# Kernel tuning notes

Hardware: AMD Instinct MI355X
Metric: run time of the kernel (lower is better)

## Reference

```python
import jax, jax.numpy as jnp
import numpy as np

B, S, D, H, H2 = 2048, 96, 7, 64, 16  # batch, seq, input/output feat, bilstm hidden, lstm2 hidden


def setup_inputs() -> dict:
    key = jax.random.key(0)
    ks = jax.random.split(key, 32)
    p = lambda i, shape: jax.random.normal(ks[i], shape, jnp.float32) * 0.1
    inp = {
        'x': jax.random.normal(ks[0], (B, S, D), jnp.float32),
        # feature attention linears (D -> D)
        'fv_w': p(1, (D, D)), 'fv_b': p(2, (D,)),
        'fk_w': p(3, (D, D)), 'fk_b': p(4, (D,)),
        'fq_w': p(5, (D, D)), 'fq_b': p(6, (D,)),
        # bidirectional LSTM, forward dir (torch layout: W_ih [4H,D], W_hh [4H,H])
        'l1f_wih': p(7, (4 * H, D)), 'l1f_whh': p(8, (4 * H, H)),
        'l1f_bih': p(9, (4 * H,)), 'l1f_bhh': p(10, (4 * H,)),
        # backward dir
        'l1b_wih': p(11, (4 * H, D)), 'l1b_whh': p(12, (4 * H, H)),
        'l1b_bih': p(13, (4 * H,)), 'l1b_bhh': p(14, (4 * H,)),
        # temporal attention linears (H -> H)
        'tv_w': p(15, (H, H)), 'tv_b': p(16, (H,)),
        'tk_w': p(17, (H, H)), 'tk_b': p(18, (H,)),
        'tq_w': p(19, (H, H)), 'tq_b': p(20, (H,)),
        # lstm2: input H=64 -> hidden H2=16
        'l2_wih': p(21, (4 * H2, H)), 'l2_whh': p(22, (4 * H2, H2)),
        'l2_bih': p(23, (4 * H2,)), 'l2_bhh': p(24, (4 * H2,)),
        # fc: 16 -> 7
        'fc_w': p(25, (D, H2)), 'fc_b': p(26, (D,)),
    }
    return inp


def _run_lstm(x, wih, whh, bih, bhh, reverse=False):
    # x: [B, S, Din]; torch gate order i, f, g, o
    Hh = whh.shape[1]
    xg = jnp.einsum('bsd,gd->sbg', x, wih) + bih + bhh  # [S, B, 4H]
    h0 = jnp.zeros((x.shape[0], Hh), x.dtype)

    def step(carry, gx):
        h, c = carry
        g = gx + h @ whh.T
        i, f, gg, o = jnp.split(g, 4, axis=-1)
        c = jax.nn.sigmoid(f) * c + jax.nn.sigmoid(i) * jnp.tanh(gg)
        h = jax.nn.sigmoid(o) * jnp.tanh(c)
        return (h, c), h

    _, hs = jax.lax.scan(step, (h0, h0), xg, reverse=reverse)
    return jnp.swapaxes(hs, 0, 1)  # [B, S, H]


def _fwd(x, fv_w, fv_b, fk_w, fk_b, fq_w, fq_b,
         l1f_wih, l1f_whh, l1f_bih, l1f_bhh,
         l1b_wih, l1b_whh, l1b_bih, l1b_bhh,
         tv_w, tv_b, tk_w, tk_b, tq_w, tq_b,
         l2_wih, l2_whh, l2_bih, l2_bhh, fc_w, fc_b):
    lin = lambda y, w, b: y @ w.T + b
    # feature attention (over the D=7 feature axis)
    v = lin(x, fv_w, fv_b)
    k = lin(x + v, fk_w, fk_b)
    q = lin(x + k, fq_w, fq_b)
    fatt = jax.nn.softmax(jnp.einsum('bsi,bsj->bij', q, k), axis=-1)  # [B, D, D]
    fa = jnp.tanh(jnp.einsum('bsi,bij->bsj', v, fatt) + x)
    # bidirectional LSTM; concat-view-mean over directions == (hf + hb) / 2
    hf = _run_lstm(fa, l1f_wih, l1f_whh, l1f_bih, l1f_bhh, reverse=False)
    hb = _run_lstm(fa, l1b_wih, l1b_whh, l1b_bih, l1b_bhh, reverse=True)
    lo = 0.5 * (hf + hb)  # [B, S, H]
    # temporal attention (over the S axis)
    tv = lin(lo, tv_w, tv_b)
    tk = lin(lo, tk_w, tk_b)
    tq = lin(lo, tq_w, tq_b)
    tatt = jax.nn.softmax(jnp.einsum('bid,bjd->bij', tq, tk), axis=-1)  # [B, S, S]
    to = jnp.tanh(jnp.einsum('bij,bjd->bid', tatt, tv))
    # second LSTM + fc
    o2 = _run_lstm(to, l2_wih, l2_whh, l2_bih, l2_bhh, reverse=False)  # [B, S, 16]
    return o2 @ fc_w.T + fc_b  # [B, S, D]


def reference(x, fv_w, fv_b, fk_w, fk_b, fq_w, fq_b,
              l1f_wih, l1f_whh, l1f_bih, l1f_bhh,
              l1b_wih, l1b_whh, l1b_bih, l1b_bhh,
              tv_w, tv_b, tk_w, tk_b, tq_w, tq_b,
              l2_wih, l2_whh, l2_bih, l2_bhh, fc_w, fc_b):
    return _fwd(x, fv_w, fv_b, fk_w, fk_b, fq_w, fq_b,
                l1f_wih, l1f_whh, l1f_bih, l1f_bhh,
                l1b_wih, l1b_whh, l1b_bih, l1b_bhh,
                tv_w, tv_b, tk_w, tk_b, tq_w, tq_b,
                l2_wih, l2_whh, l2_bih, l2_bhh, fc_w, fc_b)
```

## Files before the change

### kernel.cpp

```cpp
#include <hip/hip_runtime.h>
#include <math.h>

#define BB 2048
#define SS 96
#define DD 7
#define HH 64
#define H2 16
#define FASTR 776
#define HST2 72
#define LOST2 88
#define KST 120
#define HSB 20

typedef _Float16 f16x8 __attribute__((ext_vector_type(8)));
typedef _Float16 f16x4 __attribute__((ext_vector_type(4)));
typedef float f32x4 __attribute__((ext_vector_type(4)));

__device__ __forceinline__ float frcp(float x) { return __builtin_amdgcn_rcpf(x); }
__device__ __forceinline__ float sigm(float x) { return frcp(1.0f + __expf(-x)); }
__device__ __forceinline__ float tanh_f(float x) { return 1.0f - 2.0f * frcp(__expf(2.0f * x) + 1.0f); }
__device__ __forceinline__ float rl(float v, int l) {
    return __int_as_float(__builtin_amdgcn_readlane(__float_as_int(v), l));
}
__device__ __forceinline__ f16x8 frag_from_f32(const float* base) {
    const float4* p = (const float4*)base;
    float4 a = p[0], b = p[1];
    f16x8 r;
    r[0] = (_Float16)a.x; r[1] = (_Float16)a.y; r[2] = (_Float16)a.z; r[3] = (_Float16)a.w;
    r[4] = (_Float16)b.x; r[5] = (_Float16)b.y; r[6] = (_Float16)b.z; r[7] = (_Float16)b.w;
    return r;
}

__global__ __launch_bounds__(256) void k_feat(
    const float* __restrict__ x,
    const float* __restrict__ fv_w, const float* __restrict__ fv_b,
    const float* __restrict__ fk_w, const float* __restrict__ fk_b,
    const float* __restrict__ fq_w, const float* __restrict__ fq_b,
    float* __restrict__ fa_out)
{
    __shared__ float xs[SS * DD], vs[SS * DD], ks[SS * DD], qs[SS * DD];
    __shared__ float att[DD * DD];
    __shared__ float wv[DD * DD], wk[DD * DD], wq[DD * DD];
    __shared__ float bv[DD], bk[DD], bq[DD];
    const int b = blockIdx.x, t = threadIdx.x;
    const float* xb = x + (size_t)b * SS * DD;

    for (int idx = t; idx < SS * DD; idx += 256) xs[idx] = xb[idx];
    if (t < DD * DD) { wv[t] = fv_w[t]; wk[t] = fk_w[t]; wq[t] = fq_w[t]; }
    if (t < DD)      { bv[t] = fv_b[t]; bk[t] = fk_b[t]; bq[t] = fq_b[t]; }
    __syncthreads();

    for (int idx = t; idx < SS * DD; idx += 256) {
        int s = idx / DD, j = idx % DD;
        float a = bv[j];
        #pragma unroll
        for (int i = 0; i < DD; i++) a += xs[s * DD + i] * wv[j * DD + i];
        vs[idx] = a;
    }
    __syncthreads();
    for (int idx = t; idx < SS * DD; idx += 256) {
        int s = idx / DD, j = idx % DD;
        float a = bk[j];
        #pragma unroll
        for (int i = 0; i < DD; i++) a += (xs[s * DD + i] + vs[s * DD + i]) * wk[j * DD + i];
        ks[idx] = a;
    }
    __syncthreads();
    for (int idx = t; idx < SS * DD; idx += 256) {
        int s = idx / DD, j = idx % DD;
        float a = bq[j];
        #pragma unroll
        for (int i = 0; i < DD; i++) a += (xs[s * DD + i] + ks[s * DD + i]) * wq[j * DD + i];
        qs[idx] = a;
    }
    __syncthreads();
    if (t < DD * DD) {
        int i = t / DD, j = t % DD;
        float a = 0.0f;
        for (int s = 0; s < SS; s++) a += qs[s * DD + i] * ks[s * DD + j];
        att[t] = a;
    }
    __syncthreads();
    if (t < DD) {
        float m = -1e30f;
        #pragma unroll
        for (int j = 0; j < DD; j++) m = fmaxf(m, att[t * DD + j]);
        float e[DD]; float sum = 0.0f;
        #pragma unroll
        for (int j = 0; j < DD; j++) { e[j] = __expf(att[t * DD + j] - m); sum += e[j]; }
        float inv = frcp(sum);
        #pragma unroll
        for (int j = 0; j < DD; j++) att[t * DD + j] = e[j] * inv;
    }
    __syncthreads();
    for (int idx = t; idx < SS * DD; idx += 256) {
        int s = idx / DD, j = idx % DD;
        float a = xs[idx];
        #pragma unroll
        for (int i = 0; i < DD; i++) a += vs[s * DD + i] * att[i * DD + j];
        fa_out[(size_t)b * SS * DD + idx] = tanh_f(a);
    }
}

__global__ __launch_bounds__(256, 2) void k_bilstm(
    const float* __restrict__ fa,
    const float* __restrict__ wih_f, const float* __restrict__ whh_f,
    const float* __restrict__ bih_f, const float* __restrict__ bhh_f,
    const float* __restrict__ wih_b, const float* __restrict__ whh_b,
    const float* __restrict__ bih_b, const float* __restrict__ bhh_b,
    _Float16* __restrict__ hf, _Float16* __restrict__ hb)
{
    __shared__ _Float16 faS[16 * FASTR];
    __shared__ _Float16 hS[2][16 * HST2];

    const int bx = blockIdx.x;
    const int bg = bx >> 1, dir = bx & 1;
    const int t = threadIdx.x, lane = t & 63, w = t >> 6;
    const int col = lane & 15, quad = lane >> 4;

    const float* wih = dir ? wih_b : wih_f;
    const float* whh = dir ? whh_b : whh_f;
    const float* bih = dir ? bih_b : bih_f;
    const float* bhh = dir ? bhh_b : bhh_f;
    _Float16* hout = dir ? hb : hf;

    for (int i = t; i < 2 * 16 * HST2 / 2; i += 256) ((unsigned int*)hS)[i] = 0u;

    f16x8 wh[4][2];
    f16x8 wi[4];
    #pragma unroll
    for (int gt = 0; gt < 4; gt++) {
        const int row = 16 * (w + 4 * gt) + col;
        wh[gt][0] = frag_from_f32(whh + row * HH + quad * 8);
        wh[gt][1] = frag_from_f32(whh + row * HH + 32 + quad * 8);
        f16x8 v;
        #pragma unroll
        for (int j = 0; j < 8; j++) v[j] = (_Float16)0.0f;
        if (quad == 0) {
            #pragma unroll
            for (int j = 0; j < DD; j++) v[j] = (_Float16)wih[row * DD + j];
            v[7] = (_Float16)(bih[row] + bhh[row]);
        }
        wi[gt] = v;
    }

    const float* fab = fa + (size_t)(bg * 16) * SS * DD;
    for (int idx = t; idx < 16 * SS * DD; idx += 256) {
        int n = idx / (SS * DD), r = idx % (SS * DD);
        int s = r / DD, i = r % DD;
        faS[n * FASTR + s * 8 + i] = (_Float16)fab[idx];
    }
    for (int idx = t; idx < 16 * SS; idx += 256) {
        int n = idx / SS, s = idx % SS;
        faS[n * FASTR + s * 8 + 7] = (_Float16)1.0f;
    }
    __syncthreads();

    const int sstep = dir ? -HH : HH;
    _Float16* hp = hout + ((size_t)(bg * 16 + col)) * SS * HH
                 + (dir ? (SS - 1) : 0) * HH + 16 * w + quad * 4;

    const f32x4 ZC = {0.f, 0.f, 0.f, 0.f};
    float c0 = 0.f, c1 = 0.f, c2 = 0.f, c3 = 0.f;
    f16x4 hq;
    f32x4 gin[4];

    {
        const int s0 = dir ? (SS - 1) : 0;
        f16x8 faf;
        #pragma unroll
        for (int j = 0; j < 8; j++) faf[j] = (_Float16)0.0f;
        if (quad == 0) faf = *(const f16x8*)(&faS[col * FASTR + s0 * 8]);
        #pragma unroll
        for (int gt = 0; gt < 4; gt++)
            gin[gt] = __builtin_amdgcn_mfma_f32_16x16x32_f16(wi[gt], faf, ZC, 0, 0, 0);
    }

    for (int step = 0; step < SS; step++) {
        const int p = step & 1;

        if (step) {
            *(f16x4*)hp = hq;
            hp += sstep;
        }

        f16x8 h0 = *(const f16x8*)(&hS[p][col * HST2 + quad * 8]);
        f16x8 h1 = *(const f16x8*)(&hS[p][col * HST2 + 32 + quad * 8]);

        f32x4 g[4];
        #pragma unroll
        for (int gt = 0; gt < 4; gt++) {
            f32x4 acc = __builtin_amdgcn_mfma_f32_16x16x32_f16(wh[gt][0], h0, gin[gt], 0, 0, 0);
            acc = __builtin_amdgcn_mfma_f32_16x16x32_f16(wh[gt][1], h1, acc, 0, 0, 0);
            g[gt] = acc;
        }
        {
            float iv, fv, gv, ov, hv;
            iv = sigm(g[0][0]); fv = sigm(g[1][0]); gv = tanh_f(g[2][0]); ov = sigm(g[3][0]);
            c0 = fv * c0 + iv * gv; hv = ov * tanh_f(c0); hq[0] = (_Float16)hv;
            iv = sigm(g[0][1]); fv = sigm(g[1][1]); gv = tanh_f(g[2][1]); ov = sigm(g[3][1]);
            c1 = fv * c1 + iv * gv; hv = ov * tanh_f(c1); hq[1] = (_Float16)hv;
            iv = sigm(g[0][2]); fv = sigm(g[1][2]); gv = tanh_f(g[2][2]); ov = sigm(g[3][2]);
            c2 = fv * c2 + iv * gv; hv = ov * tanh_f(c2); hq[2] = (_Float16)hv;
            iv = sigm(g[0][3]); fv = sigm(g[1][3]); gv = tanh_f(g[2][3]); ov = sigm(g[3][3]);
            c3 = fv * c3 + iv * gv; hv = ov * tanh_f(c3); hq[3] = (_Float16)hv;
        }
        *(f16x4*)(&hS[1 - p][col * HST2 + 16 * w + quad * 4]) = hq;

        if (step + 1 < SS) {
            const int sn = dir ? (SS - 2 - step) : (step + 1);
            f16x8 faf;
            #pragma unroll
            for (int j = 0; j < 8; j++) faf[j] = (_Float16)0.0f;
            if (quad == 0) faf = *(const f16x8*)(&faS[col * FASTR + sn * 8]);
            #pragma unroll
            for (int gt = 0; gt < 4; gt++)
                gin[gt] = __builtin_amdgcn_mfma_f32_16x16x32_f16(wi[gt], faf, ZC, 0, 0, 0);
        }
        __syncthreads();
    }
    *(f16x4*)hp = hq;
}

__global__ __launch_bounds__(512, 2) void k_attn(
    const _Float16* __restrict__ hf, const _Float16* __restrict__ hb,
    const float* __restrict__ tv_w, const float* __restrict__ tv_b,
    const float* __restrict__ tk_w, const float* __restrict__ tk_b,
    const float* __restrict__ tq_w, const float* __restrict__ tq_b,
    const float* __restrict__ l2_wih,
    const float* __restrict__ l2_bih, const float* __restrict__ l2_bhh,
    _Float16* __restrict__ xg2)
{
    __shared__ _Float16 loB[SS * LOST2];
    __shared__ _Float16 qB[SS * KST];
    __shared__ _Float16 tkS[SS * KST];
    __shared__ _Float16 tvT[HH * KST];

    const int b = blockIdx.x, t = threadIdx.x;
    const int lane = t & 63, w = t >> 6;
    const int col = lane & 15, quad = lane >> 4;

    const _Float16* hfp = hf + (size_t)b * SS * HH;
    const _Float16* hbp = hb + (size_t)b * SS * HH;
    for (int g8 = t; g8 < 768; g8 += 512) {
        f16x8 va = *(const f16x8*)(hfp + g8 * 8);
        f16x8 vb = *(const f16x8*)(hbp + g8 * 8);
        int s = g8 >> 3, d = (g8 & 7) * 8;
        f16x8 r;
        #pragma unroll
        for (int j = 0; j < 8; j++) r[j] = (_Float16)(0.5f * ((float)va[j] + (float)vb[j]));
        *(f16x8*)(&loB[s * LOST2 + d]) = r;
    }
    __syncthreads();

    for (int i = 0; i < 9; i++) {
        const int flat = w + 8 * i;
        const int proj = flat / 24, rem = flat % 24;
        const int mt = rem >> 2, nt = rem & 3;
        const float* wmat = (proj == 0) ? tv_w : (proj == 1) ? tk_w : tq_w;
        const float* bvec = (proj == 0) ? tv_b : (proj == 1) ? tk_b : tq_b;
        const int j = 16 * nt + col;
        f32x4 acc = {0.f, 0.f, 0.f, 0.f};
        #pragma unroll
        for (int kc = 0; kc < 2; kc++) {
            f16x8 a  = *(const f16x8*)(&loB[(16 * mt + col) * LOST2 + kc * 32 + quad * 8]);
            f16x8 bb = frag_from_f32(wmat + j * HH + kc * 32 + quad * 8);
            acc = __builtin_amdgcn_mfma_f32_16x16x32_f16(a, bb, acc, 0, 0, 0);
        }
        const float bj = bvec[j];
        #pragma unroll
        for (int r = 0; r < 4; r++) {
            const float v = acc[r] + bj;
            const int row = 16 * mt + quad * 4 + r;
            if (proj == 0)      tvT[j * KST + row] = (_Float16)v;
            else if (proj == 1) tkS[row * KST + j] = (_Float16)v;
            else                qB[row * KST + j]  = (_Float16)v;
        }
    }
    __syncthreads();

    if (w < 6) {
        const int mt = w;
        f16x8 aq0 = *(const f16x8*)(qB + (16 * mt + col) * KST + quad * 8);
        f16x8 aq1 = *(const f16x8*)(qB + (16 * mt + col) * KST + 32 + quad * 8);
        f32x4 sc[6];
        #pragma unroll
        for (int nt = 0; nt < 6; nt++) {
            f32x4 acc = {0.f, 0.f, 0.f, 0.f};
            f16x8 b0 = *(const f16x8*)(tkS + (16 * nt + col) * KST + quad * 8);
            f16x8 b1 = *(const f16x8*)(tkS + (16 * nt + col) * KST + 32 + quad * 8);
            acc = __builtin_amdgcn_mfma_f32_16x16x32_f16(aq0, b0, acc, 0, 0, 0);
            acc = __builtin_amdgcn_mfma_f32_16x16x32_f16(aq1, b1, acc, 0, 0, 0);
            sc[nt] = acc;
        }
        #pragma unroll
        for (int r = 0; r < 4; r++) {
            float m = sc[0][r];
            #pragma unroll
            for (int nt = 1; nt < 6; nt++) m = fmaxf(m, sc[nt][r]);
            #pragma unroll
            for (int o = 1; o < 16; o <<= 1) m = fmaxf(m, __shfl_xor(m, o));
            float e[6]; float sum = 0.0f;
            #pragma unroll
            for (int nt = 0; nt < 6; nt++) { e[nt] = __expf(sc[nt][r] - m); sum += e[nt]; }
            #pragma unroll
            for (int o = 1; o < 16; o <<= 1) sum += __shfl_xor(sum, o);
            const float inv = frcp(sum);
            const int row = 16 * mt + quad * 4 + r;
            #pragma unroll
            for (int nt = 0; nt < 6; nt++)
                qB[row * KST + 16 * nt + col] = (_Float16)(e[nt] * inv);
        }
        f16x8 pa0 = *(const f16x8*)(qB + (16 * mt + col) * KST + quad * 8);
        f16x8 pa1 = *(const f16x8*)(qB + (16 * mt + col) * KST + 32 + quad * 8);
        f16x8 pa2 = *(const f16x8*)(qB + (16 * mt + col) * KST + 64 + quad * 8);
        #pragma unroll
        for (int nt = 0; nt < 4; nt++) {
            f32x4 acc = {0.f, 0.f, 0.f, 0.f};
            const _Float16* tvrow = tvT + (16 * nt + col) * KST;
            acc = __builtin_amdgcn_mfma_f32_16x16x32_f16(pa0, *(const f16x8*)(tvrow + quad * 8), acc, 0, 0, 0);
            acc = __builtin_amdgcn_mfma_f32_16x16x32_f16(pa1, *(const f16x8*)(tvrow + 32 + quad * 8), acc, 0, 0, 0);
            acc = __builtin_amdgcn_mfma_f32_16x16x32_f16(pa2, *(const f16x8*)(tvrow + 64 + quad * 8), acc, 0, 0, 0);
            #pragma unroll
            for (int r = 0; r < 4; r++)
                loB[(16 * mt + quad * 4 + r) * LOST2 + 16 * nt + col] = (_Float16)tanh_f(acc[r]);
        }
    }
    __syncthreads();

    for (int i = 0; i < 3; i++) {
        const int flat = w + 8 * i;
        const int mt = flat >> 2, nt = flat & 3;
        const int g = 16 * nt + col;
        f32x4 acc = {0.f, 0.f, 0.f, 0.f};
        #pragma unroll
        for (int kc = 0; kc < 2; kc++) {
            f16x8 a  = *(const f16x8*)(&loB[(16 * mt + col) * LOST2 + kc * 32 + quad * 8]);
            f16x8 bb = frag_from_f32(l2_wih + g * HH + kc * 32 + quad * 8);
            acc = __builtin_amdgcn_mfma_f32_16x16x32_f16(a, bb, acc, 0, 0, 0);
        }
        const float bg2 = l2_bih[g] + l2_bhh[g];
        #pragma unroll
        for (int r = 0; r < 4; r++) {
            const int row = 16 * mt + quad * 4 + r;
            xg2[(size_t)b * SS * HH + row * HH + g] = (_Float16)(acc[r] + bg2);
        }
    }
}

__global__ __launch_bounds__(256) void k_lstm2(
    const _Float16* __restrict__ xg2,
    const float* __restrict__ l2_whh,
    const float* __restrict__ fc_w, const float* __restrict__ fc_b,
    float* __restrict__ out)
{
    __shared__ _Float16 hsb[4][SS * HSB];

    const int t = threadIdx.x, lane = t & 63, w = t >> 6;
    const int n = blockIdx.x * 4 + w;
    const int u16 = lane & 15;

    float whr[H2];
    #pragma unroll
    for (int j = 0; j < H2; j++) whr[j] = l2_whh[lane * H2 + j];

    const _Float16* xgp = xg2 + (size_t)n * SS * HH + lane;
    float h = 0.0f, c = 0.0f;
    _Float16 xv = xgp[0];

    for (int s = 0; s < SS; s++) {
        _Float16 xnext = (_Float16)0.0f;
        if (s + 1 < SS) xnext = xgp[(s + 1) * HH];

        float a = (float)xv;
        #pragma unroll
        for (int j = 0; j < H2; j++) a += rl(h, j) * whr[j];
        float iv = __shfl(a, u16);
        float fv = __shfl(a, H2 + u16);
        float gv = __shfl(a, 2 * H2 + u16);
        float ov = __shfl(a, 3 * H2 + u16);
        c = sigm(fv) * c + sigm(iv) * tanh_f(gv);
        h = sigm(ov) * tanh_f(c);
        if (lane < H2) hsb[w][s * HSB + lane] = (_Float16)h;
        xv = xnext;
    }
    __syncthreads();

    for (int s = lane; s < SS; s += 64) {
        float hr[H2];
        #pragma unroll
        for (int j = 0; j < H2; j++) hr[j] = (float)hsb[w][s * HSB + j];
        float* op = out + ((size_t)n * SS + s) * DD;
        #pragma unroll
        for (int d = 0; d < DD; d++) {
            float a = fc_b[d];
            #pragma unroll
            for (int j = 0; j < H2; j++) a += hr[j] * fc_w[d * H2 + j];
            op[d] = a;
        }
    }
}

extern "C" void kernel_launch(void* const* d_in, const int* in_sizes, int n_in,
                              void* d_out, int out_size, void* d_ws, size_t ws_size,
                              hipStream_t stream) {
    const float* x     = (const float*)d_in[0];
    const float* fv_w  = (const float*)d_in[1];
    const float* fv_b  = (const float*)d_in[2];
    const float* fk_w  = (const float*)d_in[3];
    const float* fk_b  = (const float*)d_in[4];
    const float* fq_w  = (const float*)d_in[5];
    const float* fq_b  = (const float*)d_in[6];
    const float* l1f_wih = (const float*)d_in[7];
    const float* l1f_whh = (const float*)d_in[8];
    const float* l1f_bih = (const float*)d_in[9];
    const float* l1f_bhh = (const float*)d_in[10];
    const float* l1b_wih = (const float*)d_in[11];
    const float* l1b_whh = (const float*)d_in[12];
    const float* l1b_bih = (const float*)d_in[13];
    const float* l1b_bhh = (const float*)d_in[14];
    const float* tv_w  = (const float*)d_in[15];
    const float* tv_b  = (const float*)d_in[16];
    const float* tk_w  = (const float*)d_in[17];
    const float* tk_b  = (const float*)d_in[18];
    const float* tq_w  = (const float*)d_in[19];
    const float* tq_b  = (const float*)d_in[20];
    const float* l2_wih = (const float*)d_in[21];
    const float* l2_whh = (const float*)d_in[22];
    const float* l2_bih = (const float*)d_in[23];
    const float* l2_bhh = (const float*)d_in[24];
    const float* fc_w  = (const float*)d_in[25];
    const float* fc_b  = (const float*)d_in[26];

    float* fa = (float*)d_ws;
    _Float16* hf = (_Float16*)(fa + (size_t)BB * SS * DD);
    _Float16* hb = hf + (size_t)BB * SS * HH;
    _Float16* xg2 = hf;

    k_feat<<<BB, 256, 0, stream>>>(x, fv_w, fv_b, fk_w, fk_b, fq_w, fq_b, fa);
    k_bilstm<<<256, 256, 0, stream>>>(fa,
        l1f_wih, l1f_whh, l1f_bih, l1f_bhh,
        l1b_wih, l1b_whh, l1b_bih, l1b_bhh, hf, hb);
    k_attn<<<BB, 512, 0, stream>>>(hf, hb,
        tv_w, tv_b, tk_w, tk_b, tq_w, tq_b,
        l2_wih, l2_bih, l2_bhh, xg2);
    k_lstm2<<<512, 256, 0, stream>>>(xg2, l2_whh, fc_w, fc_b, (float*)d_out);
}
```

Before: 297.1 us.

## Use MFMA for LSTM2 recurrence and shrink attention LDS for occupancy

The second LSTM is rewritten so each 64-thread block handles 16 sequences and computes the recurrent gate matmul with 16x16x16 MFMA. Gate inputs are double-buffered in registers, which replaces the per-lane readlane dot products and shuffles of the old one-sequence-per-wave design. In the attention kernel, the Q/K and probability buffers share one LDS region with tighter strides, and an extra barrier makes that aliasing safe; launch bounds are raised to allow more resident blocks per CU. The risks are the extra barrier, possible LDS bank conflicts from the new strides, and much lower parallelism in lstm2, which now launches only 128 single-wave blocks.

```diff
diff --git a/kernel.cpp b/kernel.cpp
--- a/kernel.cpp
+++ b/kernel.cpp
@@ -8,9 +8,11 @@
 #define H2 16
 #define FASTR 776
 #define HST2 72
-#define LOST2 88
-#define KST 120
-#define HSB 20
+#define LO_ST 72
+#define QK_ST 68
+#define TV_ST 104
+#define P_ST 104
+#define HP 20
 
 typedef _Float16 f16x8 __attribute__((ext_vector_type(8)));
 typedef _Float16 f16x4 __attribute__((ext_vector_type(4)));
@@ -28,6 +30,14 @@
     f16x8 r;
     r[0] = (_Float16)a.x; r[1] = (_Float16)a.y; r[2] = (_Float16)a.z; r[3] = (_Float16)a.w;
     r[4] = (_Float16)b.x; r[5] = (_Float16)b.y; r[6] = (_Float16)b.z; r[7] = (_Float16)b.w;
+    return r;
+}
+__device__ __forceinline__ f16x8 ld2x4(const _Float16* p) {
+    f16x4 a = *(const f16x4*)p;
+    f16x4 b = *(const f16x4*)(p + 4);
+    f16x8 r;
+    r[0]=a[0]; r[1]=a[1]; r[2]=a[2]; r[3]=a[3];
+    r[4]=b[0]; r[5]=b[1]; r[6]=b[2]; r[7]=b[3];
     return r;
 }
 
@@ -222,7 +232,7 @@
     *(f16x4*)hp = hq;
 }
 
-__global__ __launch_bounds__(512, 2) void k_attn(
+__global__ __launch_bounds__(512, 6) void k_attn(
     const _Float16* __restrict__ hf, const _Float16* __restrict__ hb,
     const float* __restrict__ tv_w, const float* __restrict__ tv_b,
     const float* __restrict__ tk_w, const float* __restrict__ tk_b,
@@ -231,10 +241,12 @@
     const float* __restrict__ l2_bih, const float* __restrict__ l2_bhh,
     _Float16* __restrict__ xg2)
 {
-    __shared__ _Float16 loB[SS * LOST2];
-    __shared__ _Float16 qB[SS * KST];
-    __shared__ _Float16 tkS[SS * KST];
-    __shared__ _Float16 tvT[HH * KST];
+    __shared__ __align__(16) _Float16 loB[SS * LO_ST];
+    __shared__ __align__(16) _Float16 tvT[HH * TV_ST];
+    __shared__ __align__(16) _Float16 uQK[2 * SS * QK_ST];
+    _Float16* qS  = uQK;
+    _Float16* tkS = uQK + SS * QK_ST;
+    _Float16* pS  = uQK;
 
     const int b = blockIdx.x, t = threadIdx.x;
     const int lane = t & 63, w = t >> 6;
@@ -249,7 +261,7 @@
         f16x8 r;
         #pragma unroll
         for (int j = 0; j < 8; j++) r[j] = (_Float16)(0.5f * ((float)va[j] + (float)vb[j]));
-        *(f16x8*)(&loB[s * LOST2 + d]) = r;
+        *(f16x8*)(&loB[s * LO_ST + d]) = r;
     }
     __syncthreads();
 
@@ -263,7 +275,7 @@
         f32x4 acc = {0.f, 0.f, 0.f, 0.f};
         #pragma unroll
         for (int kc = 0; kc < 2; kc++) {
-            f16x8 a  = *(const f16x8*)(&loB[(16 * mt + col) * LOST2 + kc * 32 + quad * 8]);
+            f16x8 a  = *(const f16x8*)(&loB[(16 * mt + col) * LO_ST + kc * 32 + quad * 8]);
             f16x8 bb = frag_from_f32(wmat + j * HH + kc * 32 + quad * 8);
             acc = __builtin_amdgcn_mfma_f32_16x16x32_f16(a, bb, acc, 0, 0, 0);
         }
@@ -272,27 +284,31 @@
         for (int r = 0; r < 4; r++) {
             const float v = acc[r] + bj;
             const int row = 16 * mt + quad * 4 + r;
-            if (proj == 0)      tvT[j * KST + row] = (_Float16)v;
-            else if (proj == 1) tkS[row * KST + j] = (_Float16)v;
-            else                qB[row * KST + j]  = (_Float16)v;
-        }
-    }
-    __syncthreads();
-
+            if (proj == 0)      tvT[j * TV_ST + row] = (_Float16)v;
+            else if (proj == 1) tkS[row * QK_ST + j] = (_Float16)v;
+            else                qS[row * QK_ST + j]  = (_Float16)v;
+        }
+    }
+    __syncthreads();
+
+    f32x4 sc[6];
+    const int mt = w;
     if (w < 6) {
-        const int mt = w;
-        f16x8 aq0 = *(const f16x8*)(qB + (16 * mt + col) * KST + quad * 8);
-        f16x8 aq1 = *(const f16x8*)(qB + (16 * mt + col) * KST + 32 + quad * 8);
-        f32x4 sc[6];
+        f16x8 aq0 = ld2x4(qS + (16 * mt + col) * QK_ST + quad * 8);
+        f16x8 aq1 = ld2x4(qS + (16 * mt + col) * QK_ST + 32 + quad * 8);
         #pragma unroll
         for (int nt = 0; nt < 6; nt++) {
             f32x4 acc = {0.f, 0.f, 0.f, 0.f};
-            f16x8 b0 = *(const f16x8*)(tkS + (16 * nt + col) * KST + quad * 8);
-            f16x8 b1 = *(const f16x8*)(tkS + (16 * nt + col) * KST + 32 + quad * 8);
+            f16x8 b0 = ld2x4(tkS + (16 * nt + col) * QK_ST + quad * 8);
+            f16x8 b1 = ld2x4(tkS + (16 * nt + col) * QK_ST + 32 + quad * 8);
             acc = __builtin_amdgcn_mfma_f32_16x16x32_f16(aq0, b0, acc, 0, 0, 0);
             acc = __builtin_amdgcn_mfma_f32_16x16x32_f16(aq1, b1, acc, 0, 0, 0);
             sc[nt] = acc;
         }
+    }
+    __syncthreads();
+
+    if (w < 6) {
         #pragma unroll
         for (int r = 0; r < 4; r++) {
             float m = sc[0][r];
@@ -309,93 +325,145 @@
             const int row = 16 * mt + quad * 4 + r;
             #pragma unroll
             for (int nt = 0; nt < 6; nt++)
-                qB[row * KST + 16 * nt + col] = (_Float16)(e[nt] * inv);
-        }
-        f16x8 pa0 = *(const f16x8*)(qB + (16 * mt + col) * KST + quad * 8);
-        f16x8 pa1 = *(const f16x8*)(qB + (16 * mt + col) * KST + 32 + quad * 8);
-        f16x8 pa2 = *(const f16x8*)(qB + (16 * mt + col) * KST + 64 + quad * 8);
+                pS[row * P_ST + 16 * nt + col] = (_Float16)(e[nt] * inv);
+        }
+        f16x8 pa0 = *(const f16x8*)(pS + (16 * mt + col) * P_ST + quad * 8);
+        f16x8 pa1 = *(const f16x8*)(pS + (16 * mt + col) * P_ST + 32 + quad * 8);
+        f16x8 pa2 = *(const f16x8*)(pS + (16 * mt + col) * P_ST + 64 + quad * 8);
         #pragma unroll
         for (int nt = 0; nt < 4; nt++) {
             f32x4 acc = {0.f, 0.f, 0.f, 0.f};
-            const _Float16* tvrow = tvT + (16 * nt + col) * KST;
+            const _Float16* tvrow = tvT + (16 * nt + col) * TV_ST;
             acc = __builtin_amdgcn_mfma_f32_16x16x32_f16(pa0, *(const f16x8*)(tvrow + quad * 8), acc, 0, 0, 0);
             acc = __builtin_amdgcn_mfma_f32_16x16x32_f16(pa1, *(const f16x8*)(tvrow + 32 + quad * 8), acc, 0, 0, 0);
             acc = __builtin_amdgcn_mfma_f32_16x16x32_f16(pa2, *(const f16x8*)(tvrow + 64 + quad * 8), acc, 0, 0, 0);
             #pragma unroll
             for (int r = 0; r < 4; r++)
-                loB[(16 * mt + quad * 4 + r) * LOST2 + 16 * nt + col] = (_Float16)tanh_f(acc[r]);
+                loB[(16 * mt + quad * 4 + r) * LO_ST + 16 * nt + col] = (_Float16)tanh_f(acc[r]);
         }
     }
     __syncthreads();
 
     for (int i = 0; i < 3; i++) {
         const int flat = w + 8 * i;
-        const int mt = flat >> 2, nt = flat & 3;
+        const int mt2 = flat >> 2, nt = flat & 3;
         const int g = 16 * nt + col;
         f32x4 acc = {0.f, 0.f, 0.f, 0.f};
         #pragma unroll
         for (int kc = 0; kc < 2; kc++) {
-            f16x8 a  = *(const f16x8*)(&loB[(16 * mt + col) * LOST2 + kc * 32 + quad * 8]);
+            f16x8 a  = *(const f16x8*)(&loB[(16 * mt2 + col) * LO_ST + kc * 32 + quad * 8]);
             f16x8 bb = frag_from_f32(l2_wih + g * HH + kc * 32 + quad * 8);
             acc = __builtin_amdgcn_mfma_f32_16x16x32_f16(a, bb, acc, 0, 0, 0);
         }
         const float bg2 = l2_bih[g] + l2_bhh[g];
         #pragma unroll
         for (int r = 0; r < 4; r++) {
-            const int row = 16 * mt + quad * 4 + r;
+            const int row = 16 * mt2 + quad * 4 + r;
             xg2[(size_t)b * SS * HH + row * HH + g] = (_Float16)(acc[r] + bg2);
         }
     }
 }
 
-__global__ __launch_bounds__(256) void k_lstm2(
+__device__ __forceinline__ void l2_step(const f16x4* xf, const f16x4* whhA,
+                                        f16x4& hB, f32x4& c, _Float16* hdst)
+{
+    f32x4 g[4];
+    #pragma unroll
+    for (int gt = 0; gt < 4; gt++) {
+        f32x4 ci;
+        #pragma unroll
+        for (int r = 0; r < 4; r++) ci[r] = (float)xf[gt][r];
+        g[gt] = __builtin_amdgcn_mfma_f32_16x16x16f16(whhA[gt], hB, ci, 0, 0, 0);
+    }
+    #pragma unroll
+    for (int r = 0; r < 4; r++) {
+        float iv = sigm(g[0][r]), fv = sigm(g[1][r]), gv = tanh_f(g[2][r]), ov = sigm(g[3][r]);
+        c[r] = fv * c[r] + iv * gv;
+        float hv = ov * tanh_f(c[r]);
+        hB[r] = (_Float16)hv;
+    }
+    *(f16x4*)hdst = hB;
+}
+
+__global__ __launch_bounds__(64, 1) void k_lstm2(
     const _Float16* __restrict__ xg2,
     const float* __restrict__ l2_whh,
     const float* __restrict__ fc_w, const float* __restrict__ fc_b,
     float* __restrict__ out)
 {
-    __shared__ _Float16 hsb[4][SS * HSB];
-
-    const int t = threadIdx.x, lane = t & 63, w = t >> 6;
-    const int n = blockIdx.x * 4 + w;
-    const int u16 = lane & 15;
-
-    float whr[H2];
+    __shared__ __align__(16) _Float16 hS[SS * 16 * HP];
+
+    const int lane = threadIdx.x;
+    const int col = lane & 15, quad = lane >> 4;
+    const int n0 = blockIdx.x * 16;
+
+    f16x4 whhA[4];
     #pragma unroll
-    for (int j = 0; j < H2; j++) whr[j] = l2_whh[lane * H2 + j];
-
-    const _Float16* xgp = xg2 + (size_t)n * SS * HH + lane;
-    float h = 0.0f, c = 0.0f;
-    _Float16 xv = xgp[0];
-
-    for (int s = 0; s < SS; s++) {
-        _Float16 xnext = (_Float16)0.0f;
-        if (s + 1 < SS) xnext = xgp[(s + 1) * HH];
-
-        float a = (float)xv;
-        #pragma unroll
-        for (int j = 0; j < H2; j++) a += rl(h, j) * whr[j];
-        float iv = __shfl(a, u16);
-        float fv = __shfl(a, H2 + u16);
-        float gv = __shfl(a, 2 * H2 + u16);
-        float ov = __shfl(a, 3 * H2 + u16);
-        c = sigm(fv) * c + sigm(iv) * tanh_f(gv);
-        h = sigm(ov) * tanh_f(c);
-        if (lane < H2) hsb[w][s * HSB + lane] = (_Float16)h;
-        xv = xnext;
-    }
-    __syncthreads();
-
-    for (int s = lane; s < SS; s += 64) {
-        float hr[H2];
-        #pragma unroll
-        for (int j = 0; j < H2; j++) hr[j] = (float)hsb[w][s * HSB + j];
-        float* op = out + ((size_t)n * SS + s) * DD;
+    for (int gt = 0; gt < 4; gt++) {
+        const float4 wq = *(const float4*)(l2_whh + (16 * gt + col) * H2 + quad * 4);
+        f16x4 v;
+        v[0] = (_Float16)wq.x; v[1] = (_Float16)wq.y;
+        v[2] = (_Float16)wq.z; v[3] = (_Float16)wq.w;
+        whhA[gt] = v;
+    }
+
+    const _Float16* xgp = xg2 + ((size_t)(n0 + col) * SS) * HH + quad * 4;
+
+    f16x4 xA[4][4], xB[4][4];
+    #pragma unroll
+    for (int k = 0; k < 4; k++)
+        #pragma unroll
+        for (int gt = 0; gt < 4; gt++)
+            xA[k][gt] = *(const f16x4*)(xgp + (size_t)k * HH + 16 * gt);
+
+    f16x4 hB; hB[0] = hB[1] = hB[2] = hB[3] = (_Float16)0.0f;
+    f32x4 c = {0.f, 0.f, 0.f, 0.f};
+
+    for (int sb = 0; sb < SS; sb += 8) {
+        #pragma unroll
+        for (int k = 0; k < 4; k++)
+            #pragma unroll
+            for (int gt = 0; gt < 4; gt++)
+                xB[k][gt] = *(const f16x4*)(xgp + (size_t)(sb + 4 + k) * HH + 16 * gt);
+        #pragma unroll
+        for (int k = 0; k < 4; k++)
+            l2_step(xA[k], whhA, hB, c, &hS[((sb + k) * 16 + col) * HP + quad * 4]);
+        if (sb + 8 < SS) {
+            #pragma unroll
+            for (int k = 0; k < 4; k++)
+                #pragma unroll
+                for (int gt = 0; gt < 4; gt++)
+                    xA[k][gt] = *(const f16x4*)(xgp + (size_t)(sb + 8 + k) * HH + 16 * gt);
+        }
+        #pragma unroll
+        for (int k = 0; k < 4; k++)
+            l2_step(xB[k], whhA, hB, c, &hS[((sb + 4 + k) * 16 + col) * HP + quad * 4]);
+    }
+
+    float fcw[DD][H2];
+    float fcb[DD];
+    #pragma unroll
+    for (int d = 0; d < DD; d++) {
+        fcb[d] = fc_b[d];
+        #pragma unroll
+        for (int j = 0; j < H2; j++) fcw[d][j] = fc_w[d * H2 + j];
+    }
+    for (int r = lane; r < SS * 16; r += 64) {
+        const int n = r / SS, s = r % SS;
+        const _Float16* hp = &hS[(s * 16 + n) * HP];
+        float h[H2];
+        #pragma unroll
+        for (int jq = 0; jq < 4; jq++) {
+            f16x4 hv = *(const f16x4*)(hp + 4 * jq);
+            #pragma unroll
+            for (int i = 0; i < 4; i++) h[4 * jq + i] = (float)hv[i];
+        }
+        float* op = out + ((size_t)(n0 + n) * SS + s) * DD;
         #pragma unroll
         for (int d = 0; d < DD; d++) {
-            float a = fc_b[d];
-            #pragma unroll
-            for (int j = 0; j < H2; j++) a += hr[j] * fc_w[d * H2 + j];
+            float a = fcb[d];
+            #pragma unroll
+            for (int j = 0; j < H2; j++) a += h[j] * fcw[d][j];
             op[d] = a;
         }
     }
@@ -444,5 +512,5 @@
     k_attn<<<BB, 512, 0, stream>>>(hf, hb,
         tv_w, tv_b, tk_w, tk_b, tq_w, tq_b,
         l2_wih, l2_bih, l2_bhh, xg2);
-    k_lstm2<<<512, 256, 0, stream>>>(xg2, l2_whh, fc_w, fc_b, (float*)d_out);
-}
+    k_lstm2<<<BB / 16, 64, 0, stream>>>(xg2, l2_whh, fc_w, fc_b, (float*)d_out);
+}
```

Result: slower. 318.4 us (+7.2%).

## Emit padded fp16 feature output and shrink attention shared memory via aliasing

Applied to the files above, without the earlier changes.

k_feat now writes its output as fp16 in the padded 8-wide layout k_bilstm expects, with the bias-one column already filled in. k_bilstm can then copy it to shared memory with plain 16-byte vector copies instead of doing per-element conversion and index math. k_attn gets tighter shared-memory strides and aliases the probability buffer onto the Q/K buffer, with an added barrier. This cuts LDS footprint, which may allow more resident blocks, at the cost of an extra sync and split 8-byte loads for the unaligned Q/K stride.

```diff
diff --git a/kernel.cpp b/kernel.cpp
--- a/kernel.cpp
+++ b/kernel.cpp
@@ -8,8 +8,10 @@
 #define H2 16
 #define FASTR 776
 #define HST2 72
-#define LOST2 88
-#define KST 120
+#define LO_ST 72
+#define QK_ST 68
+#define TV_ST 104
+#define P_ST 104
 #define HSB 20
 
 typedef _Float16 f16x8 __attribute__((ext_vector_type(8)));
@@ -30,13 +32,21 @@
     r[4] = (_Float16)b.x; r[5] = (_Float16)b.y; r[6] = (_Float16)b.z; r[7] = (_Float16)b.w;
     return r;
 }
+__device__ __forceinline__ f16x8 ld2x4(const _Float16* p) {
+    f16x4 a = *(const f16x4*)p;
+    f16x4 b = *(const f16x4*)(p + 4);
+    f16x8 r;
+    r[0]=a[0]; r[1]=a[1]; r[2]=a[2]; r[3]=a[3];
+    r[4]=b[0]; r[5]=b[1]; r[6]=b[2]; r[7]=b[3];
+    return r;
+}
 
 __global__ __launch_bounds__(256) void k_feat(
     const float* __restrict__ x,
     const float* __restrict__ fv_w, const float* __restrict__ fv_b,
     const float* __restrict__ fk_w, const float* __restrict__ fk_b,
     const float* __restrict__ fq_w, const float* __restrict__ fq_b,
-    float* __restrict__ fa_out)
+    _Float16* __restrict__ fa16)
 {
     __shared__ float xs[SS * DD], vs[SS * DD], ks[SS * DD], qs[SS * DD];
     __shared__ float att[DD * DD];
@@ -93,25 +103,27 @@
         for (int j = 0; j < DD; j++) att[t * DD + j] = e[j] * inv;
     }
     __syncthreads();
+    _Float16* fb = fa16 + (size_t)b * FASTR;
     for (int idx = t; idx < SS * DD; idx += 256) {
         int s = idx / DD, j = idx % DD;
         float a = xs[idx];
         #pragma unroll
         for (int i = 0; i < DD; i++) a += vs[s * DD + i] * att[i * DD + j];
-        fa_out[(size_t)b * SS * DD + idx] = tanh_f(a);
-    }
+        fb[s * 8 + j] = (_Float16)tanh_f(a);
+    }
+    if (t < SS) fb[t * 8 + 7] = (_Float16)1.0f;
 }
 
 __global__ __launch_bounds__(256, 2) void k_bilstm(
-    const float* __restrict__ fa,
+    const _Float16* __restrict__ fa16,
     const float* __restrict__ wih_f, const float* __restrict__ whh_f,
     const float* __restrict__ bih_f, const float* __restrict__ bhh_f,
     const float* __restrict__ wih_b, const float* __restrict__ whh_b,
     const float* __restrict__ bih_b, const float* __restrict__ bhh_b,
     _Float16* __restrict__ hf, _Float16* __restrict__ hb)
 {
-    __shared__ _Float16 faS[16 * FASTR];
-    __shared__ _Float16 hS[2][16 * HST2];
+    __shared__ __align__(16) _Float16 faS[16 * FASTR];
+    __shared__ __align__(16) _Float16 hS[2][16 * HST2];
 
     const int bx = blockIdx.x;
     const int bg = bx >> 1, dir = bx & 1;
@@ -144,16 +156,9 @@
         wi[gt] = v;
     }
 
-    const float* fab = fa + (size_t)(bg * 16) * SS * DD;
-    for (int idx = t; idx < 16 * SS * DD; idx += 256) {
-        int n = idx / (SS * DD), r = idx % (SS * DD);
-        int s = r / DD, i = r % DD;
-        faS[n * FASTR + s * 8 + i] = (_Float16)fab[idx];
-    }
-    for (int idx = t; idx < 16 * SS; idx += 256) {
-        int n = idx / SS, s = idx % SS;
-        faS[n * FASTR + s * 8 + 7] = (_Float16)1.0f;
-    }
+    const f16x8* fab = (const f16x8*)(fa16 + (size_t)(bg * 16) * FASTR);
+    f16x8* faD = (f16x8*)faS;
+    for (int i8 = t; i8 < 16 * FASTR / 8; i8 += 256) faD[i8] = fab[i8];
     __syncthreads();
 
     const int sstep = dir ? -HH : HH;
@@ -231,10 +236,12 @@
     const float* __restrict__ l2_bih, const float* __restrict__ l2_bhh,
     _Float16* __restrict__ xg2)
 {
-    __shared__ _Float16 loB[SS * LOST2];
-    __shared__ _Float16 qB[SS * KST];
-    __shared__ _Float16 tkS[SS * KST];
-    __shared__ _Float16 tvT[HH * KST];
+    __shared__ __align__(16) _Float16 loB[SS * LO_ST];
+    __shared__ __align__(16) _Float16 tvT[HH * TV_ST];
+    __shared__ __align__(16) _Float16 uQK[2 * SS * QK_ST];
+    _Float16* qS  = uQK;
+    _Float16* tkS = uQK + SS * QK_ST;
+    _Float16* pS  = uQK;
 
     const int b = blockIdx.x, t = threadIdx.x;
     const int lane = t & 63, w = t >> 6;
@@ -249,7 +256,7 @@
         f16x8 r;
         #pragma unroll
         for (int j = 0; j < 8; j++) r[j] = (_Float16)(0.5f * ((float)va[j] + (float)vb[j]));
-        *(f16x8*)(&loB[s * LOST2 + d]) = r;
+        *(f16x8*)(&loB[s * LO_ST + d]) = r;
     }
     __syncthreads();
 
@@ -263,7 +270,7 @@
         f32x4 acc = {0.f, 0.f, 0.f, 0.f};
         #pragma unroll
         for (int kc = 0; kc < 2; kc++) {
-            f16x8 a  = *(const f16x8*)(&loB[(16 * mt + col) * LOST2 + kc * 32 + quad * 8]);
+            f16x8 a  = *(const f16x8*)(&loB[(16 * mt + col) * LO_ST + kc * 32 + quad * 8]);
             f16x8 bb = frag_from_f32(wmat + j * HH + kc * 32 + quad * 8);
             acc = __builtin_amdgcn_mfma_f32_16x16x32_f16(a, bb, acc, 0, 0, 0);
         }
@@ -272,27 +279,31 @@
         for (int r = 0; r < 4; r++) {
             const float v = acc[r] + bj;
             const int row = 16 * mt + quad * 4 + r;
-            if (proj == 0)      tvT[j * KST + row] = (_Float16)v;
-            else if (proj == 1) tkS[row * KST + j] = (_Float16)v;
-            else                qB[row * KST + j]  = (_Float16)v;
-        }
-    }
-    __syncthreads();
-
+            if (proj == 0)      tvT[j * TV_ST + row] = (_Float16)v;
+            else if (proj == 1) tkS[row * QK_ST + j] = (_Float16)v;
+            else                qS[row * QK_ST + j]  = (_Float16)v;
+        }
+    }
+    __syncthreads();
+
+    f32x4 sc[6];
+    const int mt = w;
     if (w < 6) {
-        const int mt = w;
-        f16x8 aq0 = *(const f16x8*)(qB + (16 * mt + col) * KST + quad * 8);
-        f16x8 aq1 = *(const f16x8*)(qB + (16 * mt + col) * KST + 32 + quad * 8);
-        f32x4 sc[6];
+        f16x8 aq0 = ld2x4(qS + (16 * mt + col) * QK_ST + quad * 8);
+        f16x8 aq1 = ld2x4(qS + (16 * mt + col) * QK_ST + 32 + quad * 8);
         #pragma unroll
         for (int nt = 0; nt < 6; nt++) {
             f32x4 acc = {0.f, 0.f, 0.f, 0.f};
-            f16x8 b0 = *(const f16x8*)(tkS + (16 * nt + col) * KST + quad * 8);
-            f16x8 b1 = *(const f16x8*)(tkS + (16 * nt + col) * KST + 32 + quad * 8);
+            f16x8 b0 = ld2x4(tkS + (16 * nt + col) * QK_ST + quad * 8);
+            f16x8 b1 = ld2x4(tkS + (16 * nt + col) * QK_ST + 32 + quad * 8);
             acc = __builtin_amdgcn_mfma_f32_16x16x32_f16(aq0, b0, acc, 0, 0, 0);
             acc = __builtin_amdgcn_mfma_f32_16x16x32_f16(aq1, b1, acc, 0, 0, 0);
             sc[nt] = acc;
         }
+    }
+    __syncthreads();
+
+    if (w < 6) {
         #pragma unroll
         for (int r = 0; r < 4; r++) {
             float m = sc[0][r];
@@ -309,40 +320,40 @@
             const int row = 16 * mt + quad * 4 + r;
             #pragma unroll
             for (int nt = 0; nt < 6; nt++)
-                qB[row * KST + 16 * nt + col] = (_Float16)(e[nt] * inv);
-        }
-        f16x8 pa0 = *(const f16x8*)(qB + (16 * mt + col) * KST + quad * 8);
-        f16x8 pa1 = *(const f16x8*)(qB + (16 * mt + col) * KST + 32 + quad * 8);
-        f16x8 pa2 = *(const f16x8*)(qB + (16 * mt + col) * KST + 64 + quad * 8);
+                pS[row * P_ST + 16 * nt + col] = (_Float16)(e[nt] * inv);
+        }
+        f16x8 pa0 = *(const f16x8*)(pS + (16 * mt + col) * P_ST + quad * 8);
+        f16x8 pa1 = *(const f16x8*)(pS + (16 * mt + col) * P_ST + 32 + quad * 8);
+        f16x8 pa2 = *(const f16x8*)(pS + (16 * mt + col) * P_ST + 64 + quad * 8);
         #pragma unroll
         for (int nt = 0; nt < 4; nt++) {
             f32x4 acc = {0.f, 0.f, 0.f, 0.f};
-            const _Float16* tvrow = tvT + (16 * nt + col) * KST;
+            const _Float16* tvrow = tvT + (16 * nt + col) * TV_ST;
             acc = __builtin_amdgcn_mfma_f32_16x16x32_f16(pa0, *(const f16x8*)(tvrow + quad * 8), acc, 0, 0, 0);
             acc = __builtin_amdgcn_mfma_f32_16x16x32_f16(pa1, *(const f16x8*)(tvrow + 32 + quad * 8), acc, 0, 0, 0);
             acc = __builtin_amdgcn_mfma_f32_16x16x32_f16(pa2, *(const f16x8*)(tvrow + 64 + quad * 8), acc, 0, 0, 0);
             #pragma unroll
             for (int r = 0; r < 4; r++)
-                loB[(16 * mt + quad * 4 + r) * LOST2 + 16 * nt + col] = (_Float16)tanh_f(acc[r]);
+                loB[(16 * mt + quad * 4 + r) * LO_ST + 16 * nt + col] = (_Float16)tanh_f(acc[r]);
         }
     }
     __syncthreads();
 
     for (int i = 0; i < 3; i++) {
         const int flat = w + 8 * i;
-        const int mt = flat >> 2, nt = flat & 3;
+        const int mt2 = flat >> 2, nt = flat & 3;
         const int g = 16 * nt + col;
         f32x4 acc = {0.f, 0.f, 0.f, 0.f};
         #pragma unroll
         for (int kc = 0; kc < 2; kc++) {
-            f16x8 a  = *(const f16x8*)(&loB[(16 * mt + col) * LOST2 + kc * 32 + quad * 8]);
+            f16x8 a  = *(const f16x8*)(&loB[(16 * mt2 + col) * LO_ST + kc * 32 + quad * 8]);
             f16x8 bb = frag_from_f32(l2_wih + g * HH + kc * 32 + quad * 8);
             acc = __builtin_amdgcn_mfma_f32_16x16x32_f16(a, bb, acc, 0, 0, 0);
         }
         const float bg2 = l2_bih[g] + l2_bhh[g];
         #pragma unroll
         for (int r = 0; r < 4; r++) {
-            const int row = 16 * mt + quad * 4 + r;
+            const int row = 16 * mt2 + quad * 4 + r;
             xg2[(size_t)b * SS * HH + row * HH + g] = (_Float16)(acc[r] + bg2);
         }
     }
@@ -432,13 +443,13 @@
     const float* fc_w  = (const float*)d_in[25];
     const float* fc_b  = (const float*)d_in[26];
 
-    float* fa = (float*)d_ws;
-    _Float16* hf = (_Float16*)(fa + (size_t)BB * SS * DD);
+    _Float16* fa16 = (_Float16*)d_ws;
+    _Float16* hf = fa16 + (size_t)BB * FASTR;
     _Float16* hb = hf + (size_t)BB * SS * HH;
     _Float16* xg2 = hf;
 
-    k_feat<<<BB, 256, 0, stream>>>(x, fv_w, fv_b, fk_w, fk_b, fq_w, fq_b, fa);
-    k_bilstm<<<256, 256, 0, stream>>>(fa,
+    k_feat<<<BB, 256, 0, stream>>>(x, fv_w, fv_b, fk_w, fk_b, fq_w, fq_b, fa16);
+    k_bilstm<<<256, 256, 0, stream>>>(fa16,
         l1f_wih, l1f_whh, l1f_bih, l1f_bhh,
         l1b_wih, l1b_whh, l1b_bih, l1b_bhh, hf, hb);
     k_attn<<<BB, 512, 0, stream>>>(hf, hb,
```

Result: no change. 294.6 us (-0.8%).
